# Kernel tuning notes

Measured on AMD Instinct MI355X. Metric: run time of the kernel, lower is better.

Reference implementation:

```python
import jax, jax.numpy as jnp
import numpy as np

N_NODES = 100000


def gcn_conv(x, row, col, W, b, n_nodes):
    # PyG GCNConv: add self-loops, symmetric normalization, linear, scatter-add, bias
    deg = jnp.zeros((n_nodes,), x.dtype).at[col].add(1.0)
    dinv = jnp.where(deg > 0, jax.lax.rsqrt(deg), 0.0)
    norm = dinv[row] * dinv[col]                      # [E+N]
    h = x @ W                                         # [N, out]
    msg = h[row] * norm[:, None]                      # [E+N, out]
    out = jax.ops.segment_sum(msg, col, num_segments=n_nodes)
    return out + b


def setup_inputs() -> dict:
    key = jax.random.key(0)
    ks = jax.random.split(key, 8)
    E = 1600000
    edge_index = jax.random.randint(ks[0], (2, E), 0, N_NODES, dtype=jnp.int64)
    node_features = jax.random.normal(ks[1], (N_NODES, 16), dtype=jnp.float32)
    W1 = jax.random.normal(ks[2], (16, 32), dtype=jnp.float32) * 0.25
    b1 = jnp.zeros((32,), jnp.float32)
    W2 = jax.random.normal(ks[3], (32, 16), dtype=jnp.float32) * 0.18
    b2 = jnp.zeros((16,), jnp.float32)
    fc_W = jax.random.normal(ks[4], (16, 1), dtype=jnp.float32) * 0.25
    fc_b = jnp.zeros((1,), jnp.float32)
    return {"edge_index": edge_index, "node_features": node_features,
            "W1": W1, "b1": b1, "W2": W2, "b2": b2, "fc_W": fc_W, "fc_b": fc_b}


def reference(edge_index, node_features, W1, b1, W2, b2, fc_W, fc_b):
    n = node_features.shape[0]
    loops = jnp.arange(n, dtype=edge_index.dtype)
    row = jnp.concatenate([edge_index[0], loops])     # sources (with self-loops)
    col = jnp.concatenate([edge_index[1], loops])     # targets (with self-loops)
    x = jax.nn.relu(gcn_conv(node_features, row, col, W1, b1, n))
    # F.dropout with training=False is identity (inference)
    x = jax.nn.relu(gcn_conv(x, row, col, W2, b2, n))
    return x @ fc_W + fc_b
```

## Files before the change

### kernel.cpp

```cpp
#include <hip/hip_runtime.h>
#include <hip/hip_fp16.h>


constexpr int NN  = 100000;
constexpr int FIN = 16;
constexpr int FH  = 32;
constexpr int FO  = 16;

constexpr int BK      = 256;
constexpr int NBUCKET = (NN + BK - 1) / BK;
constexpr int CHUNK   = 8192;
constexpr int CAP     = 5376;

static __device__ __forceinline__ int pack2(float a, float b) {
    __half2 t = __float22half2_rn(make_float2(a, b));
    return *reinterpret_cast<int*>(&t);
}
static __device__ __forceinline__ float2 unpack2(int v) {
    __half2 t = *reinterpret_cast<__half2*>(&v);
    return __half22float2(t);
}

__global__ void init_kernel(int* __restrict__ bcursor) {
    int b = blockIdx.x * blockDim.x + threadIdx.x;
    if (b < NBUCKET) bcursor[b] = b * CAP;
}

__global__ __launch_bounds__(256) void bucket_fill_kernel(
        const int* __restrict__ row, const int* __restrict__ col,
        int* __restrict__ bcursor, int* __restrict__ srow, int E) {
    __shared__ int bcnt[NBUCKET];
    __shared__ int bcur[NBUCKET];
    int t = threadIdx.x;
    int e0 = blockIdx.x * CHUNK;
    int m = E - e0; if (m > CHUNK) m = CHUNK;
    for (int b = t; b < NBUCKET; b += 256) bcnt[b] = 0;
    __syncthreads();
    for (int i = t; i < m; i += 256)
        atomicAdd(&bcnt[col[e0 + i] >> 8], 1);
    __syncthreads();
    for (int b = t; b < NBUCKET; b += 256) {
        int v = bcnt[b];
        bcur[b] = v ? atomicAdd(&bcursor[b], v) : 0;
    }
    __syncthreads();
    for (int i = t; i < m; i += 256) {
        int c = col[e0 + i];
        int r = row[e0 + i];
        int p = atomicAdd(&bcur[c >> 8], 1);
        srow[p] = ((c & (BK - 1)) << 17) | r;
    }
}

__global__ __launch_bounds__(256) void bucket_sort_mm1_kernel(
        const int* __restrict__ bcursor, int* __restrict__ srow,
        int* __restrict__ off, int* __restrict__ cnt, float* __restrict__ dinv,
        const float* __restrict__ x, const float* __restrict__ W1,
        __half* __restrict__ g1, int n) {
    __shared__ int ebuf[CAP];
    __shared__ int sorted[CAP];
    __shared__ int cnt2[BK];
    __shared__ int aux[BK];
    __shared__ float w1[FIN * FH];
    int t = threadIdx.x;
    for (int i = t; i < FIN * FH; i += 256) w1[i] = W1[i];
    int lo = blockIdx.x << 8;
    int nodes = n - lo; if (nodes > BK) nodes = BK;
    int s0 = blockIdx.x * CAP;
    int m = bcursor[blockIdx.x] - s0;
    if (m > CAP) m = CAP;
    for (int i = t; i < m; i += 256) ebuf[i] = srow[s0 + i];
    cnt2[t] = 0;
    __syncthreads();
    for (int i = t; i < m; i += 256) atomicAdd(&cnt2[ebuf[i] >> 17], 1);
    __syncthreads();
    int v = cnt2[t];
    aux[t] = v;
    __syncthreads();
    for (int d = 1; d < BK; d <<= 1) {
        int a = (t >= d) ? aux[t - d] : 0;
        __syncthreads();
        aux[t] += a;
        __syncthreads();
    }
    int excl = aux[t] - v;
    cnt2[t] = excl;
    float di = rsqrtf((float)v + 1.0f);
    if (t < nodes) {
        off[lo + t]  = s0 + excl;
        cnt[lo + t]  = v;
        dinv[lo + t] = di;
    }
    __syncthreads();
    for (int i = t; i < m; i += 256) {
        int pv = ebuf[i];
        int p = atomicAdd(&cnt2[pv >> 17], 1);
        sorted[p] = pv & 0x1FFFF;
    }
    __syncthreads();
    for (int i = t; i < m; i += 256) srow[s0 + i] = sorted[i];
    if (t < nodes) {
        int nd = lo + t;
        float xi[FIN];
        const float4* xv = (const float4*)(x + (long long)nd * FIN);
        #pragma unroll
        for (int i = 0; i < FIN / 4; i++) {
            float4 vv = xv[i];
            xi[4*i] = vv.x; xi[4*i+1] = vv.y; xi[4*i+2] = vv.z; xi[4*i+3] = vv.w;
        }
        float h[FH];
        #pragma unroll
        for (int j = 0; j < FH; j++) h[j] = 0.f;
        #pragma unroll
        for (int i = 0; i < FIN; i++) {
            float xs = xi[i];
            #pragma unroll
            for (int j = 0; j < FH; j++) h[j] += xs * w1[i * FH + j];
        }
        int4* gv = (int4*)(g1 + (long long)nd * FH);
        #pragma unroll
        for (int k = 0; k < 4; k++) {
            gv[k] = make_int4(pack2(h[8*k]*di,   h[8*k+1]*di),
                              pack2(h[8*k+2]*di, h[8*k+3]*di),
                              pack2(h[8*k+4]*di, h[8*k+5]*di),
                              pack2(h[8*k+6]*di, h[8*k+7]*di));
        }
    }
}

constexpr int XS = 36;
__global__ __launch_bounds__(256) void gather_mm2_kernel(
        const int* __restrict__ off, const int* __restrict__ cnt,
        const int* __restrict__ srow, const __half* __restrict__ g1,
        const float* __restrict__ dinv, const float* __restrict__ b1,
        const float* __restrict__ W2, __half* __restrict__ g2, int n) {
    __shared__ float xs[64 * XS];
    __shared__ float w[FH * FO];
    __shared__ float bb[FH];
    int t = threadIdx.x;
    for (int i = t; i < FH * FO; i += 256) w[i] = W2[i];
    if (t < FH) bb[t] = b1[t];
    int nl = t >> 2;
    int q = t & 3;
    int node = blockIdx.x * 64 + nl;
    bool live = node < n;
    float acc[8] = {0.f,0.f,0.f,0.f,0.f,0.f,0.f,0.f};
    float di = 0.f;
    if (live) {
        di = dinv[node];
        {
            int4 raw = ((const int4*)(g1 + (long long)node * FH))[q];
            float2 f0 = unpack2(raw.x), f1 = unpack2(raw.y);
            float2 f2 = unpack2(raw.z), f3 = unpack2(raw.w);
            acc[0] = f0.x; acc[1] = f0.y; acc[2] = f1.x; acc[3] = f1.y;
            acc[4] = f2.x; acc[5] = f2.y; acc[6] = f3.x; acc[7] = f3.y;
        }
        int s = off[node];
        int m = cnt[node];
        int i = 0;
        for (; i + 3 < m; i += 4) {
            int r0 = srow[s + i];
            int r1 = srow[s + i + 1];
            int r2 = srow[s + i + 2];
            int r3 = srow[s + i + 3];
            int4 ra = ((const int4*)(g1 + (long long)r0 * FH))[q];
            int4 rb = ((const int4*)(g1 + (long long)r1 * FH))[q];
            int4 rc = ((const int4*)(g1 + (long long)r2 * FH))[q];
            int4 rd = ((const int4*)(g1 + (long long)r3 * FH))[q];
            float2 u;
            u = unpack2(ra.x); acc[0] += u.x; acc[1] += u.y;
            u = unpack2(ra.y); acc[2] += u.x; acc[3] += u.y;
            u = unpack2(ra.z); acc[4] += u.x; acc[5] += u.y;
            u = unpack2(ra.w); acc[6] += u.x; acc[7] += u.y;
            u = unpack2(rb.x); acc[0] += u.x; acc[1] += u.y;
            u = unpack2(rb.y); acc[2] += u.x; acc[3] += u.y;
            u = unpack2(rb.z); acc[4] += u.x; acc[5] += u.y;
            u = unpack2(rb.w); acc[6] += u.x; acc[7] += u.y;
            u = unpack2(rc.x); acc[0] += u.x; acc[1] += u.y;
            u = unpack2(rc.y); acc[2] += u.x; acc[3] += u.y;
            u = unpack2(rc.z); acc[4] += u.x; acc[5] += u.y;
            u = unpack2(rc.w); acc[6] += u.x; acc[7] += u.y;
            u = unpack2(rd.x); acc[0] += u.x; acc[1] += u.y;
            u = unpack2(rd.y); acc[2] += u.x; acc[3] += u.y;
            u = unpack2(rd.z); acc[4] += u.x; acc[5] += u.y;
            u = unpack2(rd.w); acc[6] += u.x; acc[7] += u.y;
        }
        for (; i < m; i++) {
            int r0 = srow[s + i];
            int4 ra = ((const int4*)(g1 + (long long)r0 * FH))[q];
            float2 u;
            u = unpack2(ra.x); acc[0] += u.x; acc[1] += u.y;
            u = unpack2(ra.y); acc[2] += u.x; acc[3] += u.y;
            u = unpack2(ra.z); acc[4] += u.x; acc[5] += u.y;
            u = unpack2(ra.w); acc[6] += u.x; acc[7] += u.y;
        }
    }
    __syncthreads();
    if (live) {
        float* xr = xs + nl * XS + 8 * q;
        #pragma unroll
        for (int j = 0; j < 8; j++) {
            float a = acc[j] * di + bb[8*q + j];
            xr[j] = a > 0.f ? a : 0.f;
        }
    }
    __syncthreads();
    if (live) {
        const float* xr = xs + nl * XS;
        int k0 = 4 * q;
        float o0 = 0.f, o1 = 0.f, o2 = 0.f, o3 = 0.f;
        #pragma unroll
        for (int j = 0; j < FH; j++) {
            float xj = xr[j];
            const float* wr = w + j * FO + k0;
            o0 += xj * wr[0];
            o1 += xj * wr[1];
            o2 += xj * wr[2];
            o3 += xj * wr[3];
        }
        ((int2*)(g2 + (long long)node * FO))[q] =
            make_int2(pack2(o0 * di, o1 * di), pack2(o2 * di, o3 * di));
    }
}

__global__ __launch_bounds__(256) void gather_fc_kernel(
        const int* __restrict__ off, const int* __restrict__ cnt,
        const int* __restrict__ srow, const __half* __restrict__ g2,
        const float* __restrict__ dinv, const float* __restrict__ b2,
        const float* __restrict__ fcW, const float* __restrict__ fcb,
        float* __restrict__ out, int n) {
    __shared__ float w[FO];
    __shared__ float bb[FO];
    __shared__ float fb;
    int t = threadIdx.x;
    if (t < FO) { w[t] = fcW[t]; bb[t] = b2[t]; }
    if (t == 0) fb = fcb[0];
    __syncthreads();
    int node = blockIdx.x * 128 + (t >> 1);
    int q = t & 1;
    if (node >= n) return;
    float di = dinv[node];
    float acc[8];
    {
        int4 raw = ((const int4*)(g2 + (long long)node * FO))[q];
        float2 f0 = unpack2(raw.x), f1 = unpack2(raw.y);
        float2 f2 = unpack2(raw.z), f3 = unpack2(raw.w);
        acc[0] = f0.x; acc[1] = f0.y; acc[2] = f1.x; acc[3] = f1.y;
        acc[4] = f2.x; acc[5] = f2.y; acc[6] = f3.x; acc[7] = f3.y;
    }
    int s = off[node];
    int m = cnt[node];
    int i = 0;
    for (; i + 3 < m; i += 4) {
        int r0 = srow[s + i];
        int r1 = srow[s + i + 1];
        int r2 = srow[s + i + 2];
        int r3 = srow[s + i + 3];
        int4 ra = ((const int4*)(g2 + (long long)r0 * FO))[q];
        int4 rb = ((const int4*)(g2 + (long long)r1 * FO))[q];
        int4 rc = ((const int4*)(g2 + (long long)r2 * FO))[q];
        int4 rd = ((const int4*)(g2 + (long long)r3 * FO))[q];
        float2 u;
        u = unpack2(ra.x); acc[0] += u.x; acc[1] += u.y;
        u = unpack2(ra.y); acc[2] += u.x; acc[3] += u.y;
        u = unpack2(ra.z); acc[4] += u.x; acc[5] += u.y;
        u = unpack2(ra.w); acc[6] += u.x; acc[7] += u.y;
        u = unpack2(rb.x); acc[0] += u.x; acc[1] += u.y;
        u = unpack2(rb.y); acc[2] += u.x; acc[3] += u.y;
        u = unpack2(rb.z); acc[4] += u.x; acc[5] += u.y;
        u = unpack2(rb.w); acc[6] += u.x; acc[7] += u.y;
        u = unpack2(rc.x); acc[0] += u.x; acc[1] += u.y;
        u = unpack2(rc.y); acc[2] += u.x; acc[3] += u.y;
        u = unpack2(rc.z); acc[4] += u.x; acc[5] += u.y;
        u = unpack2(rc.w); acc[6] += u.x; acc[7] += u.y;
        u = unpack2(rd.x); acc[0] += u.x; acc[1] += u.y;
        u = unpack2(rd.y); acc[2] += u.x; acc[3] += u.y;
        u = unpack2(rd.z); acc[4] += u.x; acc[5] += u.y;
        u = unpack2(rd.w); acc[6] += u.x; acc[7] += u.y;
    }
    for (; i < m; i++) {
        int r0 = srow[s + i];
        int4 ra = ((const int4*)(g2 + (long long)r0 * FO))[q];
        float2 u;
        u = unpack2(ra.x); acc[0] += u.x; acc[1] += u.y;
        u = unpack2(ra.y); acc[2] += u.x; acc[3] += u.y;
        u = unpack2(ra.z); acc[4] += u.x; acc[5] += u.y;
        u = unpack2(ra.w); acc[6] += u.x; acc[7] += u.y;
    }
    float p = 0.f;
    #pragma unroll
    for (int j = 0; j < 8; j++) {
        float a = acc[j] * di + bb[8*q + j];
        p += (a > 0.f ? a : 0.f) * w[8*q + j];
    }
    p += __shfl_down(p, 1, 2);
    if (q == 0) out[node] = p + fb;
}

extern "C" void kernel_launch(void* const* d_in, const int* in_sizes, int n_in,
                              void* d_out, int out_size, void* d_ws, size_t ws_size,
                              hipStream_t stream) {
    const int*   edge = (const int*)d_in[0];
    const float* x    = (const float*)d_in[1];
    const float* W1   = (const float*)d_in[2];
    const float* b1   = (const float*)d_in[3];
    const float* W2   = (const float*)d_in[4];
    const float* b2   = (const float*)d_in[5];
    const float* fcW  = (const float*)d_in[6];
    const float* fcb  = (const float*)d_in[7];
    float* out = (float*)d_out;

    const int E = in_sizes[0] / 2;
    const int n = NN;
    const int* row = edge;
    const int* col = edge + E;

    const size_t nA = (size_t)((n + 127) & ~127);
    char* wsb = (char*)d_ws;
    int*   cnt     = (int*)wsb;
    int*   off     = cnt + nA;
    float* dinv    = (float*)(off + nA);
    int*   bcursor = (int*)(dinv + nA);
    int*   srow    = bcursor + 512;
    int*   srowEnd = srow + (size_t)(NBUCKET + 1) * CAP;
    __half* g1     = (__half*)srowEnd;
    __half* g2     = g1 + (size_t)n * FH;

    const int B = 256;
    const int nChunkBlocks = (E + CHUNK - 1) / CHUNK;

    init_kernel<<<2, B, 0, stream>>>(bcursor);
    bucket_fill_kernel<<<nChunkBlocks, B, 0, stream>>>(row, col, bcursor, srow, E);
    bucket_sort_mm1_kernel<<<NBUCKET, B, 0, stream>>>(bcursor, srow, off, cnt, dinv, x, W1, g1, n);
    gather_mm2_kernel<<<(n + 63) / 64, B, 0, stream>>>(off, cnt, srow, g1, dinv, b1, W2, g2, n);
    gather_fc_kernel<<<(n + 127) / 128, B, 0, stream>>>(off, cnt, srow, g2, dinv, b2, fcW, fcb, out, n);
}
```

Measured before the change: 153.5 us.

## Sort nodes by degree within buckets to balance gather loops; cache col in LDS

Each 256-node bucket now builds a counting sort of its nodes by in-degree (capped at 63) into a perm array. Both gather kernels process nodes in that permuted order, so lanes in a wavefront have similar edge counts and diverge less inside the neighbor loops. The bucket-fill kernel also keeps col in shared memory to avoid reading it twice, and halves CHUNK so the added LDS buffer fits. The cost is an extra perm indirection, scattered output writes and more, smaller fill blocks doing more global cursor atomics.

After: 161.1 us. 4.9% more time.

```diff
diff --git a/kernel.cpp b/kernel.cpp
--- a/kernel.cpp
+++ b/kernel.cpp
@@ -9,7 +9,7 @@
 
 constexpr int BK      = 256;
 constexpr int NBUCKET = (NN + BK - 1) / BK;
-constexpr int CHUNK   = 8192;
+constexpr int CHUNK   = 4096;
 constexpr int CAP     = 5376;
 
 static __device__ __forceinline__ int pack2(float a, float b) {
@@ -29,6 +29,7 @@
 __global__ __launch_bounds__(256) void bucket_fill_kernel(
         const int* __restrict__ row, const int* __restrict__ col,
         int* __restrict__ bcursor, int* __restrict__ srow, int E) {
+    __shared__ int cbuf[CHUNK];
     __shared__ int bcnt[NBUCKET];
     __shared__ int bcur[NBUCKET];
     int t = threadIdx.x;
@@ -36,8 +37,11 @@
     int m = E - e0; if (m > CHUNK) m = CHUNK;
     for (int b = t; b < NBUCKET; b += 256) bcnt[b] = 0;
     __syncthreads();
-    for (int i = t; i < m; i += 256)
-        atomicAdd(&bcnt[col[e0 + i] >> 8], 1);
+    for (int i = t; i < m; i += 256) {
+        int c = col[e0 + i];
+        cbuf[i] = c;
+        atomicAdd(&bcnt[c >> 8], 1);
+    }
     __syncthreads();
     for (int b = t; b < NBUCKET; b += 256) {
         int v = bcnt[b];
@@ -45,7 +49,7 @@
     }
     __syncthreads();
     for (int i = t; i < m; i += 256) {
-        int c = col[e0 + i];
+        int c = cbuf[i];
         int r = row[e0 + i];
         int p = atomicAdd(&bcur[c >> 8], 1);
         srow[p] = ((c & (BK - 1)) << 17) | r;
@@ -55,6 +59,7 @@
 __global__ __launch_bounds__(256) void bucket_sort_mm1_kernel(
         const int* __restrict__ bcursor, int* __restrict__ srow,
         int* __restrict__ off, int* __restrict__ cnt, float* __restrict__ dinv,
+        int* __restrict__ perm,
         const float* __restrict__ x, const float* __restrict__ W1,
         __half* __restrict__ g1, int n) {
     __shared__ int ebuf[CAP];
@@ -62,6 +67,9 @@
     __shared__ int cnt2[BK];
     __shared__ int aux[BK];
     __shared__ float w1[FIN * FH];
+    __shared__ int dcnt[64];
+    __shared__ int daux[64];
+    __shared__ int dbase[64];
     int t = threadIdx.x;
     for (int i = t; i < FIN * FH; i += 256) w1[i] = W1[i];
     int lo = blockIdx.x << 8;
@@ -71,6 +79,7 @@
     if (m > CAP) m = CAP;
     for (int i = t; i < m; i += 256) ebuf[i] = srow[s0 + i];
     cnt2[t] = 0;
+    if (t < 64) dcnt[t] = 0;
     __syncthreads();
     for (int i = t; i < m; i += 256) atomicAdd(&cnt2[ebuf[i] >> 17], 1);
     __syncthreads();
@@ -91,6 +100,23 @@
         cnt[lo + t]  = v;
         dinv[lo + t] = di;
     }
+    int key = v < 63 ? v : 63;
+    if (t < nodes) atomicAdd(&dcnt[key], 1);
+    __syncthreads();
+    if (t < 64) daux[t] = dcnt[t];
+    __syncthreads();
+    for (int d = 1; d < 64; d <<= 1) {
+        int a = (t >= d && t < 64) ? daux[t - d] : 0;
+        __syncthreads();
+        if (t < 64) daux[t] += a;
+        __syncthreads();
+    }
+    if (t < 64) dbase[t] = daux[t] - dcnt[t];
+    __syncthreads();
+    if (t < nodes) {
+        int rank = atomicAdd(&dbase[key], 1);
+        perm[lo + rank] = lo + t;
+    }
     __syncthreads();
     for (int i = t; i < m; i += 256) {
         int pv = ebuf[i];
@@ -133,7 +159,8 @@
         const int* __restrict__ off, const int* __restrict__ cnt,
         const int* __restrict__ srow, const __half* __restrict__ g1,
         const float* __restrict__ dinv, const float* __restrict__ b1,
-        const float* __restrict__ W2, __half* __restrict__ g2, int n) {
+        const float* __restrict__ W2, const int* __restrict__ perm,
+        __half* __restrict__ g2, int n) {
     __shared__ float xs[64 * XS];
     __shared__ float w[FH * FO];
     __shared__ float bb[FH];
@@ -142,8 +169,9 @@
     if (t < FH) bb[t] = b1[t];
     int nl = t >> 2;
     int q = t & 3;
-    int node = blockIdx.x * 64 + nl;
-    bool live = node < n;
+    int slot = blockIdx.x * 64 + nl;
+    bool live = slot < n;
+    int node = live ? perm[slot] : 0;
     float acc[8] = {0.f,0.f,0.f,0.f,0.f,0.f,0.f,0.f};
     float di = 0.f;
     if (live) {
@@ -228,7 +256,7 @@
         const int* __restrict__ srow, const __half* __restrict__ g2,
         const float* __restrict__ dinv, const float* __restrict__ b2,
         const float* __restrict__ fcW, const float* __restrict__ fcb,
-        float* __restrict__ out, int n) {
+        const int* __restrict__ perm, float* __restrict__ out, int n) {
     __shared__ float w[FO];
     __shared__ float bb[FO];
     __shared__ float fb;
@@ -236,9 +264,10 @@
     if (t < FO) { w[t] = fcW[t]; bb[t] = b2[t]; }
     if (t == 0) fb = fcb[0];
     __syncthreads();
-    int node = blockIdx.x * 128 + (t >> 1);
+    int slot = blockIdx.x * 128 + (t >> 1);
     int q = t & 1;
-    if (node >= n) return;
+    if (slot >= n) return;
+    int node = perm[slot];
     float di = dinv[node];
     float acc[8];
     {
@@ -320,7 +349,8 @@
     int*   cnt     = (int*)wsb;
     int*   off     = cnt + nA;
     float* dinv    = (float*)(off + nA);
-    int*   bcursor = (int*)(dinv + nA);
+    int*   perm    = (int*)(dinv + nA);
+    int*   bcursor = perm + nA;
     int*   srow    = bcursor + 512;
     int*   srowEnd = srow + (size_t)(NBUCKET + 1) * CAP;
     __half* g1     = (__half*)srowEnd;
@@ -331,7 +361,7 @@
 
     init_kernel<<<2, B, 0, stream>>>(bcursor);
     bucket_fill_kernel<<<nChunkBlocks, B, 0, stream>>>(row, col, bcursor, srow, E);
-    bucket_sort_mm1_kernel<<<NBUCKET, B, 0, stream>>>(bcursor, srow, off, cnt, dinv, x, W1, g1, n);
-    gather_mm2_kernel<<<(n + 63) / 64, B, 0, stream>>>(off, cnt, srow, g1, dinv, b1, W2, g2, n);
-    gather_fc_kernel<<<(n + 127) / 128, B, 0, stream>>>(off, cnt, srow, g2, dinv, b2, fcW, fcb, out, n);
-}
+    bucket_sort_mm1_kernel<<<NBUCKET, B, 0, stream>>>(bcursor, srow, off, cnt, dinv, perm, x, W1, g1, n);
+    gather_mm2_kernel<<<(n + 63) / 64, B, 0, stream>>>(off, cnt, srow, g1, dinv, b1, W2, perm, g2, n);
+    gather_fc_kernel<<<(n + 127) / 128, B, 0, stream>>>(off, cnt, srow, g2, dinv, b2, fcW, fcb, perm, out, n);
+}
```

## Replace bucketed two-pass sort with global histogram, scan, and atomic scatter CSR build

Applied to the files above, without the earlier changes.

Replaces the shared-memory bucket fill plus per-bucket local sort with a global per-node histogram via atomics, a per-block wave-shuffle scan fused with the first matmul, and a direct atomic scatter of source indices into per-node slots. The aim is to drop the staging pass through shared memory and the extra write-back of sorted buckets. In exchange it relies on global atomics on 100k counters and produces scattered writes, and edges within a node now land in nondeterministic order. It still assumes each 256-node bucket fits within CAP.

New measurement: 305.9 us. +99.2%, slower.

```diff
diff --git a/kernel.cpp b/kernel.cpp
--- a/kernel.cpp
+++ b/kernel.cpp
@@ -9,7 +9,6 @@
 
 constexpr int BK      = 256;
 constexpr int NBUCKET = (NN + BK - 1) / BK;
-constexpr int CHUNK   = 8192;
 constexpr int CAP     = 5376;
 
 static __device__ __forceinline__ int pack2(float a, float b) {
@@ -21,84 +20,58 @@
     return __half22float2(t);
 }
 
-__global__ void init_kernel(int* __restrict__ bcursor) {
-    int b = blockIdx.x * blockDim.x + threadIdx.x;
-    if (b < NBUCKET) bcursor[b] = b * CAP;
-}
-
-__global__ __launch_bounds__(256) void bucket_fill_kernel(
-        const int* __restrict__ row, const int* __restrict__ col,
-        int* __restrict__ bcursor, int* __restrict__ srow, int E) {
-    __shared__ int bcnt[NBUCKET];
-    __shared__ int bcur[NBUCKET];
-    int t = threadIdx.x;
-    int e0 = blockIdx.x * CHUNK;
-    int m = E - e0; if (m > CHUNK) m = CHUNK;
-    for (int b = t; b < NBUCKET; b += 256) bcnt[b] = 0;
-    __syncthreads();
-    for (int i = t; i < m; i += 256)
-        atomicAdd(&bcnt[col[e0 + i] >> 8], 1);
-    __syncthreads();
-    for (int b = t; b < NBUCKET; b += 256) {
-        int v = bcnt[b];
-        bcur[b] = v ? atomicAdd(&bcursor[b], v) : 0;
-    }
-    __syncthreads();
-    for (int i = t; i < m; i += 256) {
-        int c = col[e0 + i];
-        int r = row[e0 + i];
-        int p = atomicAdd(&bcur[c >> 8], 1);
-        srow[p] = ((c & (BK - 1)) << 17) | r;
-    }
-}
-
-__global__ __launch_bounds__(256) void bucket_sort_mm1_kernel(
-        const int* __restrict__ bcursor, int* __restrict__ srow,
-        int* __restrict__ off, int* __restrict__ cnt, float* __restrict__ dinv,
+__global__ __launch_bounds__(256) void hist_kernel(
+        const int* __restrict__ col, int* __restrict__ cnt, int E) {
+    int tid = blockIdx.x * blockDim.x + threadIdx.x;
+    int E4 = E >> 2;
+    const int4* c4 = (const int4*)col;
+    if (tid < E4) {
+        int4 c = c4[tid];
+        atomicAdd(&cnt[c.x], 1);
+        atomicAdd(&cnt[c.y], 1);
+        atomicAdd(&cnt[c.z], 1);
+        atomicAdd(&cnt[c.w], 1);
+    }
+    if (tid == 0)
+        for (int e = E4 << 2; e < E; e++) atomicAdd(&cnt[col[e]], 1);
+}
+
+__global__ __launch_bounds__(256) void scan_mm1_kernel(
+        const int* __restrict__ cnt, int* __restrict__ off,
+        int* __restrict__ cursor, float* __restrict__ dinv,
         const float* __restrict__ x, const float* __restrict__ W1,
         __half* __restrict__ g1, int n) {
-    __shared__ int ebuf[CAP];
-    __shared__ int sorted[CAP];
-    __shared__ int cnt2[BK];
-    __shared__ int aux[BK];
     __shared__ float w1[FIN * FH];
+    __shared__ int wsum[4];
+    __shared__ int wbase[4];
     int t = threadIdx.x;
     for (int i = t; i < FIN * FH; i += 256) w1[i] = W1[i];
     int lo = blockIdx.x << 8;
     int nodes = n - lo; if (nodes > BK) nodes = BK;
+    int v = (t < nodes) ? cnt[lo + t] : 0;
+    int s = v;
+    #pragma unroll
+    for (int d = 1; d < 64; d <<= 1) {
+        int u = __shfl_up(s, d, 64);
+        if ((t & 63) >= d) s += u;
+    }
+    if ((t & 63) == 63) wsum[t >> 6] = s;
+    __syncthreads();
+    if (t < 4) {
+        int b = 0;
+        for (int k = 0; k < t; k++) b += wsum[k];
+        wbase[t] = b;
+    }
+    __syncthreads();
+    int excl = s + wbase[t >> 6] - v;
     int s0 = blockIdx.x * CAP;
-    int m = bcursor[blockIdx.x] - s0;
-    if (m > CAP) m = CAP;
-    for (int i = t; i < m; i += 256) ebuf[i] = srow[s0 + i];
-    cnt2[t] = 0;
-    __syncthreads();
-    for (int i = t; i < m; i += 256) atomicAdd(&cnt2[ebuf[i] >> 17], 1);
-    __syncthreads();
-    int v = cnt2[t];
-    aux[t] = v;
-    __syncthreads();
-    for (int d = 1; d < BK; d <<= 1) {
-        int a = (t >= d) ? aux[t - d] : 0;
-        __syncthreads();
-        aux[t] += a;
-        __syncthreads();
-    }
-    int excl = aux[t] - v;
-    cnt2[t] = excl;
     float di = rsqrtf((float)v + 1.0f);
     if (t < nodes) {
-        off[lo + t]  = s0 + excl;
-        cnt[lo + t]  = v;
-        dinv[lo + t] = di;
-    }
-    __syncthreads();
-    for (int i = t; i < m; i += 256) {
-        int pv = ebuf[i];
-        int p = atomicAdd(&cnt2[pv >> 17], 1);
-        sorted[p] = pv & 0x1FFFF;
-    }
-    __syncthreads();
-    for (int i = t; i < m; i += 256) srow[s0 + i] = sorted[i];
+        off[lo + t]    = s0 + excl;
+        cursor[lo + t] = s0 + excl;
+        dinv[lo + t]   = di;
+    }
+    __syncthreads();
     if (t < nodes) {
         int nd = lo + t;
         float xi[FIN];
@@ -126,6 +99,26 @@
                               pack2(h[8*k+6]*di, h[8*k+7]*di));
         }
     }
+}
+
+__global__ __launch_bounds__(256) void scatter_kernel(
+        const int* __restrict__ row, const int* __restrict__ col,
+        int* __restrict__ cursor, int* __restrict__ srow, int E) {
+    int tid = blockIdx.x * blockDim.x + threadIdx.x;
+    int E4 = E >> 2;
+    const int4* c4 = (const int4*)col;
+    const int4* r4 = (const int4*)row;
+    if (tid < E4) {
+        int4 c = c4[tid];
+        int4 r = r4[tid];
+        srow[atomicAdd(&cursor[c.x], 1)] = r.x;
+        srow[atomicAdd(&cursor[c.y], 1)] = r.y;
+        srow[atomicAdd(&cursor[c.z], 1)] = r.z;
+        srow[atomicAdd(&cursor[c.w], 1)] = r.w;
+    }
+    if (tid == 0)
+        for (int e = E4 << 2; e < E; e++)
+            srow[atomicAdd(&cursor[col[e]], 1)] = row[e];
 }
 
 constexpr int XS = 36;
@@ -319,19 +312,21 @@
     char* wsb = (char*)d_ws;
     int*   cnt     = (int*)wsb;
     int*   off     = cnt + nA;
-    float* dinv    = (float*)(off + nA);
-    int*   bcursor = (int*)(dinv + nA);
-    int*   srow    = bcursor + 512;
+    int*   cursor  = off + nA;
+    float* dinv    = (float*)(cursor + nA);
+    int*   srow    = (int*)(dinv + nA);
     int*   srowEnd = srow + (size_t)(NBUCKET + 1) * CAP;
     __half* g1     = (__half*)srowEnd;
     __half* g2     = g1 + (size_t)n * FH;
 
     const int B = 256;
-    const int nChunkBlocks = (E + CHUNK - 1) / CHUNK;
-
-    init_kernel<<<2, B, 0, stream>>>(bcursor);
-    bucket_fill_kernel<<<nChunkBlocks, B, 0, stream>>>(row, col, bcursor, srow, E);
-    bucket_sort_mm1_kernel<<<NBUCKET, B, 0, stream>>>(bcursor, srow, off, cnt, dinv, x, W1, g1, n);
+    const int E4 = E >> 2;
+    const int nEdgeBlocks = (E4 + B - 1) / B;
+
+    hipMemsetAsync(cnt, 0, (size_t)n * sizeof(int), stream);
+    hist_kernel<<<nEdgeBlocks, B, 0, stream>>>(col, cnt, E);
+    scan_mm1_kernel<<<NBUCKET, B, 0, stream>>>(cnt, off, cursor, dinv, x, W1, g1, n);
+    scatter_kernel<<<nEdgeBlocks, B, 0, stream>>>(row, col, cursor, srow, E);
     gather_mm2_kernel<<<(n + 63) / 64, B, 0, stream>>>(off, cnt, srow, g1, dinv, b1, W2, g2, n);
     gather_fc_kernel<<<(n + 127) / 128, B, 0, stream>>>(off, cnt, srow, g2, dinv, b2, fcW, fcb, out, n);
 }
```

## Fuse bucket sort into layer-2 gather, compute degrees via global atomics

Applied to the files above, without the earlier changes.

Halves the bucket size to 128 nodes and moves the in-bucket counting sort into the layer-2 gather kernel, so the gather reads neighbor indices from shared memory instead of global srow. Degrees are now counted with global atomics during bucket fill, which lets the first matmul run as its own simple per-node kernel. The 32x16 matmul now uses per-thread partial sums combined with cross-lane shuffles instead of a shared staging buffer. In exchange there are extra global atomics per edge, a memset, and a fixed bucket capacity that silently drops edges if a bucket overflows.

After: 209.4 us. 1.36x slower.

```diff
diff --git a/kernel.cpp b/kernel.cpp
--- a/kernel.cpp
+++ b/kernel.cpp
@@ -7,10 +7,10 @@
 constexpr int FH  = 32;
 constexpr int FO  = 16;
 
-constexpr int BK      = 256;
+constexpr int BK      = 128;
 constexpr int NBUCKET = (NN + BK - 1) / BK;
 constexpr int CHUNK   = 8192;
-constexpr int CAP     = 5376;
+constexpr int CAP     = 2816;
 
 static __device__ __forceinline__ int pack2(float a, float b) {
     __half2 t = __float22half2_rn(make_float2(a, b));
@@ -28,7 +28,9 @@
 
 __global__ __launch_bounds__(256) void bucket_fill_kernel(
         const int* __restrict__ row, const int* __restrict__ col,
-        int* __restrict__ bcursor, int* __restrict__ srow, int E) {
+        int* __restrict__ bcursor, int* __restrict__ srow,
+        int* __restrict__ cnt, int E) {
+    __shared__ int cbuf[CHUNK];
     __shared__ int bcnt[NBUCKET];
     __shared__ int bcur[NBUCKET];
     int t = threadIdx.x;
@@ -36,8 +38,12 @@
     int m = E - e0; if (m > CHUNK) m = CHUNK;
     for (int b = t; b < NBUCKET; b += 256) bcnt[b] = 0;
     __syncthreads();
-    for (int i = t; i < m; i += 256)
-        atomicAdd(&bcnt[col[e0 + i] >> 8], 1);
+    for (int i = t; i < m; i += 256) {
+        int c = col[e0 + i];
+        cbuf[i] = c;
+        atomicAdd(&bcnt[c >> 7], 1);
+        atomicAdd(&cnt[c], 1);
+    }
     __syncthreads();
     for (int b = t; b < NBUCKET; b += 256) {
         int v = bcnt[b];
@@ -45,109 +51,119 @@
     }
     __syncthreads();
     for (int i = t; i < m; i += 256) {
-        int c = col[e0 + i];
+        int c = cbuf[i];
         int r = row[e0 + i];
-        int p = atomicAdd(&bcur[c >> 8], 1);
-        srow[p] = ((c & (BK - 1)) << 17) | r;
-    }
-}
-
-__global__ __launch_bounds__(256) void bucket_sort_mm1_kernel(
-        const int* __restrict__ bcursor, int* __restrict__ srow,
-        int* __restrict__ off, int* __restrict__ cnt, float* __restrict__ dinv,
+        int b = c >> 7;
+        int p = atomicAdd(&bcur[b], 1);
+        if (p < (b + 1) * CAP)
+            srow[p] = ((c & (BK - 1)) << 17) | r;
+    }
+}
+
+__global__ __launch_bounds__(256) void mm1_kernel(
+        const int* __restrict__ cnt, float* __restrict__ dinv,
         const float* __restrict__ x, const float* __restrict__ W1,
         __half* __restrict__ g1, int n) {
+    __shared__ float w1[FIN * FH];
+    int t = threadIdx.x;
+    for (int i = t; i < FIN * FH; i += 256) w1[i] = W1[i];
+    __syncthreads();
+    int nd = blockIdx.x * 256 + t;
+    if (nd >= n) return;
+    float di = rsqrtf((float)cnt[nd] + 1.0f);
+    dinv[nd] = di;
+    float xi[FIN];
+    const float4* xv = (const float4*)(x + (long long)nd * FIN);
+    #pragma unroll
+    for (int i = 0; i < FIN / 4; i++) {
+        float4 vv = xv[i];
+        xi[4*i] = vv.x; xi[4*i+1] = vv.y; xi[4*i+2] = vv.z; xi[4*i+3] = vv.w;
+    }
+    float h[FH];
+    #pragma unroll
+    for (int j = 0; j < FH; j++) h[j] = 0.f;
+    #pragma unroll
+    for (int i = 0; i < FIN; i++) {
+        float xs = xi[i];
+        #pragma unroll
+        for (int j = 0; j < FH; j++) h[j] += xs * w1[i * FH + j];
+    }
+    int4* gv = (int4*)(g1 + (long long)nd * FH);
+    #pragma unroll
+    for (int k = 0; k < 4; k++) {
+        gv[k] = make_int4(pack2(h[8*k]*di,   h[8*k+1]*di),
+                          pack2(h[8*k+2]*di, h[8*k+3]*di),
+                          pack2(h[8*k+4]*di, h[8*k+5]*di),
+                          pack2(h[8*k+6]*di, h[8*k+7]*di));
+    }
+}
+
+__global__ __launch_bounds__(512) void sortgather_mm2_kernel(
+        const int* __restrict__ bcursor, int* __restrict__ srow,
+        int* __restrict__ off,
+        const __half* __restrict__ g1, const float* __restrict__ b1,
+        const float* __restrict__ W2, __half* __restrict__ g2, int n) {
     __shared__ int ebuf[CAP];
     __shared__ int sorted[CAP];
     __shared__ int cnt2[BK];
-    __shared__ int aux[BK];
-    __shared__ float w1[FIN * FH];
+    __shared__ int noff[BK];
+    __shared__ int ncnt[BK];
+    __shared__ float sdi[BK];
+    __shared__ int wsum[2];
+    __shared__ int wbase[2];
+    __shared__ float w[FH * FO];
+    __shared__ float bb[FH];
     int t = threadIdx.x;
-    for (int i = t; i < FIN * FH; i += 256) w1[i] = W1[i];
-    int lo = blockIdx.x << 8;
+    for (int i = t; i < FH * FO; i += 512) w[i] = W2[i];
+    if (t < FH) bb[t] = b1[t];
+    int b  = blockIdx.x;
+    int lo = b << 7;
     int nodes = n - lo; if (nodes > BK) nodes = BK;
-    int s0 = blockIdx.x * CAP;
-    int m = bcursor[blockIdx.x] - s0;
+    int s0 = b * CAP;
+    int m = bcursor[b] - s0;
     if (m > CAP) m = CAP;
-    for (int i = t; i < m; i += 256) ebuf[i] = srow[s0 + i];
-    cnt2[t] = 0;
-    __syncthreads();
-    for (int i = t; i < m; i += 256) atomicAdd(&cnt2[ebuf[i] >> 17], 1);
-    __syncthreads();
-    int v = cnt2[t];
-    aux[t] = v;
-    __syncthreads();
-    for (int d = 1; d < BK; d <<= 1) {
-        int a = (t >= d) ? aux[t - d] : 0;
-        __syncthreads();
-        aux[t] += a;
-        __syncthreads();
-    }
-    int excl = aux[t] - v;
-    cnt2[t] = excl;
-    float di = rsqrtf((float)v + 1.0f);
-    if (t < nodes) {
-        off[lo + t]  = s0 + excl;
-        cnt[lo + t]  = v;
-        dinv[lo + t] = di;
-    }
-    __syncthreads();
-    for (int i = t; i < m; i += 256) {
+    if (m < 0)  m = 0;
+    for (int i = t; i < m; i += 512) ebuf[i] = srow[s0 + i];
+    if (t < BK) cnt2[t] = 0;
+    __syncthreads();
+    for (int i = t; i < m; i += 512) atomicAdd(&cnt2[ebuf[i] >> 17], 1);
+    __syncthreads();
+    int v = 0, s = 0;
+    if (t < BK) {
+        v = cnt2[t];
+        s = v;
+        #pragma unroll
+        for (int d = 1; d < 64; d <<= 1) {
+            int u = __shfl_up(s, d, 64);
+            if ((t & 63) >= d) s += u;
+        }
+        if ((t & 63) == 63) wsum[t >> 6] = s;
+    }
+    __syncthreads();
+    if (t < 2) wbase[t] = (t == 0) ? 0 : wsum[0];
+    __syncthreads();
+    if (t < BK) {
+        int excl = s + wbase[t >> 6] - v;
+        noff[t] = excl;
+        ncnt[t] = v;
+        cnt2[t] = excl;
+        sdi[t]  = rsqrtf((float)v + 1.0f);
+        if (t < nodes) off[lo + t] = s0 + excl;
+    }
+    __syncthreads();
+    for (int i = t; i < m; i += 512) {
         int pv = ebuf[i];
         int p = atomicAdd(&cnt2[pv >> 17], 1);
         sorted[p] = pv & 0x1FFFF;
     }
     __syncthreads();
-    for (int i = t; i < m; i += 256) srow[s0 + i] = sorted[i];
-    if (t < nodes) {
-        int nd = lo + t;
-        float xi[FIN];
-        const float4* xv = (const float4*)(x + (long long)nd * FIN);
-        #pragma unroll
-        for (int i = 0; i < FIN / 4; i++) {
-            float4 vv = xv[i];
-            xi[4*i] = vv.x; xi[4*i+1] = vv.y; xi[4*i+2] = vv.z; xi[4*i+3] = vv.w;
-        }
-        float h[FH];
-        #pragma unroll
-        for (int j = 0; j < FH; j++) h[j] = 0.f;
-        #pragma unroll
-        for (int i = 0; i < FIN; i++) {
-            float xs = xi[i];
-            #pragma unroll
-            for (int j = 0; j < FH; j++) h[j] += xs * w1[i * FH + j];
-        }
-        int4* gv = (int4*)(g1 + (long long)nd * FH);
-        #pragma unroll
-        for (int k = 0; k < 4; k++) {
-            gv[k] = make_int4(pack2(h[8*k]*di,   h[8*k+1]*di),
-                              pack2(h[8*k+2]*di, h[8*k+3]*di),
-                              pack2(h[8*k+4]*di, h[8*k+5]*di),
-                              pack2(h[8*k+6]*di, h[8*k+7]*di));
-        }
-    }
-}
-
-constexpr int XS = 36;
-__global__ __launch_bounds__(256) void gather_mm2_kernel(
-        const int* __restrict__ off, const int* __restrict__ cnt,
-        const int* __restrict__ srow, const __half* __restrict__ g1,
-        const float* __restrict__ dinv, const float* __restrict__ b1,
-        const float* __restrict__ W2, __half* __restrict__ g2, int n) {
-    __shared__ float xs[64 * XS];
-    __shared__ float w[FH * FO];
-    __shared__ float bb[FH];
-    int t = threadIdx.x;
-    for (int i = t; i < FH * FO; i += 256) w[i] = W2[i];
-    if (t < FH) bb[t] = b1[t];
+    for (int i = t; i < m; i += 512) srow[s0 + i] = sorted[i];
     int nl = t >> 2;
-    int q = t & 3;
-    int node = blockIdx.x * 64 + nl;
-    bool live = node < n;
-    float acc[8] = {0.f,0.f,0.f,0.f,0.f,0.f,0.f,0.f};
-    float di = 0.f;
-    if (live) {
-        di = dinv[node];
+    int q  = t & 3;
+    if (nl < nodes) {
+        int node = lo + nl;
+        float di = sdi[nl];
+        float acc[8];
         {
             int4 raw = ((const int4*)(g1 + (long long)node * FH))[q];
             float2 f0 = unpack2(raw.x), f1 = unpack2(raw.y);
@@ -155,14 +171,14 @@
             acc[0] = f0.x; acc[1] = f0.y; acc[2] = f1.x; acc[3] = f1.y;
             acc[4] = f2.x; acc[5] = f2.y; acc[6] = f3.x; acc[7] = f3.y;
         }
-        int s = off[node];
-        int m = cnt[node];
+        int sA = noff[nl];
+        int md = ncnt[nl];
         int i = 0;
-        for (; i + 3 < m; i += 4) {
-            int r0 = srow[s + i];
-            int r1 = srow[s + i + 1];
-            int r2 = srow[s + i + 2];
-            int r3 = srow[s + i + 3];
+        for (; i + 3 < md; i += 4) {
+            int r0 = sorted[sA + i];
+            int r1 = sorted[sA + i + 1];
+            int r2 = sorted[sA + i + 2];
+            int r3 = sorted[sA + i + 3];
             int4 ra = ((const int4*)(g1 + (long long)r0 * FH))[q];
             int4 rb = ((const int4*)(g1 + (long long)r1 * FH))[q];
             int4 rc = ((const int4*)(g1 + (long long)r2 * FH))[q];
@@ -185,8 +201,8 @@
             u = unpack2(rd.z); acc[4] += u.x; acc[5] += u.y;
             u = unpack2(rd.w); acc[6] += u.x; acc[7] += u.y;
         }
-        for (; i < m; i++) {
-            int r0 = srow[s + i];
+        for (; i < md; i++) {
+            int r0 = sorted[sA + i];
             int4 ra = ((const int4*)(g1 + (long long)r0 * FH))[q];
             float2 u;
             u = unpack2(ra.x); acc[0] += u.x; acc[1] += u.y;
@@ -194,32 +210,24 @@
             u = unpack2(ra.z); acc[4] += u.x; acc[5] += u.y;
             u = unpack2(ra.w); acc[6] += u.x; acc[7] += u.y;
         }
-    }
-    __syncthreads();
-    if (live) {
-        float* xr = xs + nl * XS + 8 * q;
+        float o[FO];
+        #pragma unroll
+        for (int k = 0; k < FO; k++) o[k] = 0.f;
         #pragma unroll
         for (int j = 0; j < 8; j++) {
             float a = acc[j] * di + bb[8*q + j];
-            xr[j] = a > 0.f ? a : 0.f;
-        }
-    }
-    __syncthreads();
-    if (live) {
-        const float* xr = xs + nl * XS;
-        int k0 = 4 * q;
-        float o0 = 0.f, o1 = 0.f, o2 = 0.f, o3 = 0.f;
-        #pragma unroll
-        for (int j = 0; j < FH; j++) {
-            float xj = xr[j];
-            const float* wr = w + j * FO + k0;
-            o0 += xj * wr[0];
-            o1 += xj * wr[1];
-            o2 += xj * wr[2];
-            o3 += xj * wr[3];
-        }
+            float xj = a > 0.f ? a : 0.f;
+            const float* wr = w + (8*q + j) * FO;
+            #pragma unroll
+            for (int k = 0; k < FO; k++) o[k] += xj * wr[k];
+        }
+        #pragma unroll
+        for (int k = 0; k < FO; k++) o[k] += __shfl_xor(o[k], 1);
+        #pragma unroll
+        for (int k = 0; k < FO; k++) o[k] += __shfl_xor(o[k], 2);
         ((int2*)(g2 + (long long)node * FO))[q] =
-            make_int2(pack2(o0 * di, o1 * di), pack2(o2 * di, o3 * di));
+            make_int2(pack2(o[4*q] * di,   o[4*q+1] * di),
+                      pack2(o[4*q+2] * di, o[4*q+3] * di));
     }
 }
 
@@ -321,7 +329,7 @@
     int*   off     = cnt + nA;
     float* dinv    = (float*)(off + nA);
     int*   bcursor = (int*)(dinv + nA);
-    int*   srow    = bcursor + 512;
+    int*   srow    = bcursor + 1024;
     int*   srowEnd = srow + (size_t)(NBUCKET + 1) * CAP;
     __half* g1     = (__half*)srowEnd;
     __half* g2     = g1 + (size_t)n * FH;
@@ -329,9 +337,10 @@
     const int B = 256;
     const int nChunkBlocks = (E + CHUNK - 1) / CHUNK;
 
-    init_kernel<<<2, B, 0, stream>>>(bcursor);
-    bucket_fill_kernel<<<nChunkBlocks, B, 0, stream>>>(row, col, bcursor, srow, E);
-    bucket_sort_mm1_kernel<<<NBUCKET, B, 0, stream>>>(bcursor, srow, off, cnt, dinv, x, W1, g1, n);
-    gather_mm2_kernel<<<(n + 63) / 64, B, 0, stream>>>(off, cnt, srow, g1, dinv, b1, W2, g2, n);
+    hipMemsetAsync(cnt, 0, (size_t)n * sizeof(int), stream);
+    init_kernel<<<(NBUCKET + B - 1) / B, B, 0, stream>>>(bcursor);
+    bucket_fill_kernel<<<nChunkBlocks, B, 0, stream>>>(row, col, bcursor, srow, cnt, E);
+    mm1_kernel<<<(n + B - 1) / B, B, 0, stream>>>(cnt, dinv, x, W1, g1, n);
+    sortgather_mm2_kernel<<<NBUCKET, 512, 0, stream>>>(bcursor, srow, off, g1, b1, W2, g2, n);
     gather_fc_kernel<<<(n + 127) / 128, B, 0, stream>>>(off, cnt, srow, g2, dinv, b2, fcW, fcb, out, n);
 }
```
